# Performance work log

Hardware: AMD Instinct MI355X
Metric: run time of the kernel (lower is better)

The kernel has to match this reference:

```python
import jax, jax.numpy as jnp
import numpy as np

DIM = 1024
HEADS = 16
DIM_HEAD = 64
INNER = HEADS * DIM_HEAD  # 1024
SCALE = DIM_HEAD ** -0.5


def setup_inputs() -> dict:
    key = jax.random.key(0)
    k1, k2, k3, k4 = jax.random.split(key, 4)
    x = jax.random.normal(k1, (2, 2048, DIM), dtype=jnp.float32)
    # nn.Linear(dim, inner*3, bias=False): weight [3*inner, dim]; store transposed [dim, 3*inner]
    w_qkv = jax.random.normal(k2, (DIM, 3 * INNER), dtype=jnp.float32) * (DIM ** -0.5)
    w_out = jax.random.normal(k3, (INNER, DIM), dtype=jnp.float32) * (INNER ** -0.5)
    b_out = jax.random.normal(k4, (DIM,), dtype=jnp.float32) * 0.02
    return {"x": x, "w_qkv": w_qkv, "w_out": w_out, "b_out": b_out}


def _attention(x, w_qkv, w_out, b_out):
    b, n, _ = x.shape
    qkv = x @ w_qkv  # [b, n, 3*inner]
    q_chunk = qkv[..., :INNER]  # NOTE: source bug — q, k, v all come from chunk 0
    def split_heads(t):
        return t.reshape(b, n, HEADS, DIM_HEAD).transpose(0, 2, 1, 3)  # b h n d
    q = split_heads(q_chunk) * SCALE
    k = split_heads(q_chunk)
    v = split_heads(q_chunk)
    dots = jnp.einsum('bhid,bhjd->bhij', q, k)
    mask_value = -jnp.finfo(dots.dtype).max
    causal_mask = jnp.triu(jnp.ones((n, n), dtype=bool), k=1)
    dots = jnp.where(causal_mask, mask_value, dots)
    attn = jax.nn.softmax(dots, axis=-1)
    out = jnp.einsum('bhij,bhjd->bhid', attn, v)
    out = out.transpose(0, 2, 1, 3).reshape(b, n, INNER)
    return out @ w_out + b_out


def reference(x, w_qkv, w_out, b_out):
    return _attention(x, w_qkv, w_out, b_out)
```

## Files before the change

### kernel.cpp

```cpp
#include <hip/hip_runtime.h>
#include <hip/hip_bf16.h>

typedef __attribute__((ext_vector_type(8))) short short8;
typedef __attribute__((ext_vector_type(4))) short bf16x4;
typedef __attribute__((ext_vector_type(4))) float floatx4;

#define MFMA16(a, b, c) __builtin_amdgcn_mfma_f32_16x16x32_bf16((a), (b), (c), 0, 0, 0)

#if defined(__HIP_DEVICE_COMPILE__)
  #if __has_builtin(__builtin_amdgcn_mfma_f32_16x16x16bf16_1k)
    #define MFMA_PV(a, b, c) __builtin_amdgcn_mfma_f32_16x16x16bf16_1k((a), (b), (c), 0, 0, 0)
  #elif __has_builtin(__builtin_amdgcn_mfma_f32_16x16x16_bf16)
    #define MFMA_PV(a, b, c) __builtin_amdgcn_mfma_f32_16x16x16_bf16((a), (b), (c), 0, 0, 0)
  #else
    #error "no 16x16x16 bf16 MFMA builtin found on device pass"
  #endif
#else
  #define MFMA_PV(a, b, c) (c)
#endif

#define SEQ    2048
#define DIMM   1024
#define HEADS  16
#define DHEAD  64
#define ROWS   4096
#define K1 0.18033688011112043f
#define K2 (-34.62468098133512f)


__global__ void cvt_bf16_kernel(const float* __restrict__ src,
                                __hip_bfloat16* __restrict__ dst) {
    const size_t i = (size_t)(blockIdx.x * 256 + threadIdx.x) * 4;
    floatx4 v = *(const floatx4*)(src + i);
    union { bf16x4 s; __hip_bfloat16 h[4]; } u;
#pragma unroll
    for (int j = 0; j < 4; j++) u.h[j] = __float2bfloat16(v[j]);
    *(bf16x4*)(dst + i) = u.s;
}

__global__ __launch_bounds__(256) void transpose_cvt2_kernel(
    const float* __restrict__ W1, __hip_bfloat16* __restrict__ WT1,
    const float* __restrict__ W2, __hip_bfloat16* __restrict__ WT2) {
    __shared__ __hip_bfloat16 tile[64][72];
    const float* W        = blockIdx.z ? W2 : W1;
    __hip_bfloat16* WT    = blockIdx.z ? WT2 : WT1;
    const int ld          = blockIdx.z ? DIMM : 3 * DIMM;
    const int tid = threadIdx.x;
    const int r = tid >> 2, c0 = (tid & 3) * 16;
    const int k0 = blockIdx.x * 64;
    const int n0 = blockIdx.y * 64;
    const float* src = W + (size_t)(k0 + r) * ld + n0 + c0;
    union { short8 v; __hip_bfloat16 h[8]; } a0, a1;
#pragma unroll
    for (int j = 0; j < 8; j++) {
        a0.h[j] = __float2bfloat16(src[j]);
        a1.h[j] = __float2bfloat16(src[8 + j]);
    }
    *(short8*)&tile[r][c0]     = a0.v;
    *(short8*)&tile[r][c0 + 8] = a1.v;
    __syncthreads();
    union { short8 v; __hip_bfloat16 h[8]; } u0, u1;
#pragma unroll
    for (int j = 0; j < 8; j++) {
        u0.h[j] = tile[c0 + j][r];
        u1.h[j] = tile[c0 + 8 + j][r];
    }
    __hip_bfloat16* dst = WT + (size_t)(n0 + r) * 1024 + k0 + c0;
    *(short8*)dst       = u0.v;
    *(short8*)(dst + 8) = u1.v;
}

__global__ __launch_bounds__(256) void transpose_t_kernel(
    const __hip_bfloat16* __restrict__ t,
    __hip_bfloat16* __restrict__ Tt) {
    __shared__ __hip_bfloat16 tile[64][72];
    const int tid = threadIdx.x;
    const int r = tid >> 2, c0 = (tid & 3) * 16;
    const int row0 = blockIdx.x * 64;
    const int col0 = blockIdx.y * 64;
    const __hip_bfloat16* src = t + (size_t)(row0 + r) * DIMM + col0 + c0;
    *(short8*)&tile[r][c0]     = *(const short8*)src;
    *(short8*)&tile[r][c0 + 8] = *(const short8*)(src + 8);
    __syncthreads();
    const int cb = (c0 >> 4) * 4;
    union { short8 v; __hip_bfloat16 h[8]; } u0, u1;
#pragma unroll
    for (int j = 0; j < 8; j++) {
        u0.h[j] = tile[(j >> 2) * 16 + cb + (j & 3)][r];
        u1.h[j] = tile[((j >> 2) + 2) * 16 + cb + (j & 3)][r];
    }
    __hip_bfloat16* dst = Tt + (size_t)(col0 + r) * ROWS + row0 + c0;
    *(short8*)dst       = u0.v;
    *(short8*)(dst + 8) = u1.v;
}

template <typename CT>
__global__ __launch_bounds__(256) void gemm_bf_kernel(
    const __hip_bfloat16* __restrict__ A,
    const __hip_bfloat16* __restrict__ BT,
    const float* __restrict__ bias,
    CT* __restrict__ C, int M, int N, int K) {
    __shared__ __align__(16) __hip_bfloat16 As[2][64][68];
    __shared__ __align__(16) __hip_bfloat16 Bs[2][64][68];

    const int tid  = threadIdx.x;
    const int lane = tid & 63, wid = tid >> 6;
    const int wm   = wid >> 1, wn = wid & 1;
    const int quad = lane >> 4, l15 = lane & 15;
    const int bm = blockIdx.y * 64, bn = blockIdx.x * 64;

    floatx4 acc[2][2];
#pragma unroll
    for (int r = 0; r < 2; r++)
#pragma unroll
        for (int c = 0; c < 2; c++) acc[r][c] = (floatx4){0.f, 0.f, 0.f, 0.f};

    const int sr = tid >> 2, sc = (tid & 3) * 16;
    short8 ra[2], rb[2];
    auto load_tile = [&](int k0) {
        const __hip_bfloat16* pa = A + (size_t)(bm + sr) * K + k0 + sc;
        ra[0] = *(const short8*)pa; ra[1] = *(const short8*)(pa + 8);
        const __hip_bfloat16* pb = BT + (size_t)(bn + sr) * K + k0 + sc;
        rb[0] = *(const short8*)pb; rb[1] = *(const short8*)(pb + 8);
    };
    auto store_tile = [&](int buf) {
        *(short8*)&As[buf][sr][sc]     = ra[0];
        *(short8*)&As[buf][sr][sc + 8] = ra[1];
        *(short8*)&Bs[buf][sr][sc]     = rb[0];
        *(short8*)&Bs[buf][sr][sc + 8] = rb[1];
    };

    load_tile(0);
    store_tile(0);
    if (K > 64) load_tile(64);
    __syncthreads();

    const int nk = K >> 6;
    for (int kb = 0; kb < nk; ++kb) {
        const int buf = kb & 1;
#pragma unroll
        for (int ks = 0; ks < 2; ks++) {
            short8 af[2], bf[2];
#pragma unroll
            for (int r = 0; r < 2; r++)
                af[r] = *(const short8*)&As[buf][wm * 32 + r * 16 + l15][ks * 32 + quad * 8];
#pragma unroll
            for (int c = 0; c < 2; c++)
                bf[c] = *(const short8*)&Bs[buf][wn * 32 + c * 16 + l15][ks * 32 + quad * 8];
#pragma unroll
            for (int r = 0; r < 2; r++)
#pragma unroll
                for (int c = 0; c < 2; c++)
                    acc[r][c] = MFMA16(af[r], bf[c], acc[r][c]);
        }
        if (kb + 1 < nk) store_tile(buf ^ 1);
        if (kb + 2 < nk) load_tile((kb + 2) << 6);
        __syncthreads();
    }

#pragma unroll
    for (int c = 0; c < 2; c++) {
        const int col = bn + wn * 32 + c * 16 + l15;
        const float bv = bias ? bias[col] : 0.f;
#pragma unroll
        for (int r = 0; r < 2; r++) {
            const int row0 = bm + wm * 32 + r * 16 + quad * 4;
#pragma unroll
            for (int i = 0; i < 4; i++) {
                const float v = acc[r][c][i] + bv;
                if constexpr (__is_same(CT, float))
                    C[(size_t)(row0 + i) * N + col] = v;
                else
                    C[(size_t)(row0 + i) * N + col] = __float2bfloat16(v);
            }
        }
    }
}

template <typename AT, typename CT>
__global__ __launch_bounds__(256) void gemm_fp_kernel(
    const AT* __restrict__ A, const float* __restrict__ B,
    const float* __restrict__ bias, CT* __restrict__ C,
    int M, int N, int K, int ldb) {
    __shared__ __align__(16) __hip_bfloat16 As[2][64][40];
    __shared__ __align__(16) __hip_bfloat16 Bs[2][128][40];
    const int tid = threadIdx.x;
    const int lane = tid & 63, wid = tid >> 6;
    const int wm = wid >> 1, wn = wid & 1;
    const int quad = lane >> 4, l15 = lane & 15;
    const int bm = blockIdx.y * 64, bn = blockIdx.x * 128;
    floatx4 acc[2][4];
#pragma unroll
    for (int r = 0; r < 2; r++)
#pragma unroll
        for (int c = 0; c < 4; c++) acc[r][c] = (floatx4){0.f, 0.f, 0.f, 0.f};
    const int a_lr = tid >> 2, a_lc = (tid & 3) * 8;
    const int b_kr = tid & 31, b_nc = (tid >> 5) * 16;
    floatx4 raf0, raf1; short8 rab; floatx4 rb[4];
    auto load_tile = [&](int k0) {
        const AT* pa = A + (size_t)(bm + a_lr) * K + k0 + a_lc;
        if constexpr (__is_same(AT, float)) {
            raf0 = *(const floatx4*)pa; raf1 = *(const floatx4*)(pa + 4);
        } else { rab = *(const short8*)pa; }
        const float* pb = B + (size_t)(k0 + b_kr) * ldb + bn + b_nc;
#pragma unroll
        for (int q = 0; q < 4; q++) rb[q] = *(const floatx4*)(pb + 4 * q);
    };
    auto store_tile = [&](int buf) {
        if constexpr (__is_same(AT, float)) {
            __align__(16) __hip_bfloat16 hh[8];
#pragma unroll
            for (int j = 0; j < 4; j++) {
                hh[j] = __float2bfloat16(raf0[j]); hh[4 + j] = __float2bfloat16(raf1[j]);
            }
            *(short8*)&As[buf][a_lr][a_lc] = *(short8*)&hh[0];
        } else { *(short8*)&As[buf][a_lr][a_lc] = rab; }
#pragma unroll
        for (int q = 0; q < 4; q++)
#pragma unroll
            for (int j = 0; j < 4; j++)
                Bs[buf][b_nc + 4 * q + j][b_kr] = __float2bfloat16(rb[q][j]);
    };
    load_tile(0); store_tile(0);
    if (K > 32) load_tile(32);
    __syncthreads();
    const int nk = K >> 5;
    for (int kb = 0; kb < nk; ++kb) {
        const int buf = kb & 1;
        short8 af[2], bf[4];
#pragma unroll
        for (int r = 0; r < 2; r++)
            af[r] = *(const short8*)&As[buf][wm * 32 + r * 16 + l15][quad * 8];
#pragma unroll
        for (int c = 0; c < 4; c++)
            bf[c] = *(const short8*)&Bs[buf][wn * 64 + c * 16 + l15][quad * 8];
#pragma unroll
        for (int r = 0; r < 2; r++)
#pragma unroll
            for (int c = 0; c < 4; c++)
                acc[r][c] = MFMA16(af[r], bf[c], acc[r][c]);
        if (kb + 1 < nk) store_tile(buf ^ 1);
        if (kb + 2 < nk) load_tile((kb + 2) << 5);
        __syncthreads();
    }
#pragma unroll
    for (int c = 0; c < 4; c++) {
        const int col = bn + wn * 64 + c * 16 + l15;
        const float bv = bias ? bias[col] : 0.f;
#pragma unroll
        for (int r = 0; r < 2; r++) {
            const int row0 = bm + wm * 32 + r * 16 + quad * 4;
#pragma unroll
            for (int i = 0; i < 4; i++) {
                const float v = acc[r][c][i] + bv;
                if constexpr (__is_same(CT, float)) C[(size_t)(row0 + i) * N + col] = v;
                else C[(size_t)(row0 + i) * N + col] = __float2bfloat16(v);
            }
        }
    }
}

__global__ __launch_bounds__(256) void attn_kernel(
    const __hip_bfloat16* __restrict__ T,
    const __hip_bfloat16* __restrict__ Tt,
    __hip_bfloat16* __restrict__ O) {
    __shared__ __align__(16) __hip_bfloat16 Ks[2][64][72];
    __shared__ __align__(16) __hip_bfloat16 Vt[2][64][72];

    const int tid  = threadIdx.x;
    const int lane = tid & 63, wid = tid >> 6;
    const int quad = lane >> 4, l15 = lane & 15;

    const int bx = blockIdx.x;
    const int half = bx >> 9, idx = bx & 511;
    const int g = idx & 15, h = (idx >> 4) & 15, b = idx >> 8;
    const int qt = half ? g : 31 - g;

    const size_t rowbase = (size_t)b * SEQ;
    const int hoff  = h * DHEAD;
    const int qrow0 = qt * 64;

    short8 qf[2];
    {
        const __hip_bfloat16* qp =
            T + (rowbase + qrow0 + wid * 16 + l15) * DIMM + hoff + quad * 8;
        qf[0] = *(const short8*)qp;
        qf[1] = *(const short8*)(qp + 32);
    }

    float l_lane = 0.f;
    floatx4 accO[4];
#pragma unroll
    for (int dt = 0; dt < 4; dt++) accO[dt] = (floatx4){0.f,0.f,0.f,0.f};

    const int sr = tid >> 2;
    const int sc = (tid & 3) * 16;

    short8 rK0, rK1, rV0, rV1;
    auto load_tile = [&](int kt) {
        const __hip_bfloat16* pK = T + (rowbase + kt * 64 + sr) * DIMM + hoff + sc;
        rK0 = *(const short8*)pK; rK1 = *(const short8*)(pK + 8);
        const __hip_bfloat16* pV =
            Tt + (size_t)(hoff + sr) * ROWS + rowbase + kt * 64 + sc;
        rV0 = *(const short8*)pV; rV1 = *(const short8*)(pV + 8);
    };
    auto store_tile = [&](int buf) {
        *(short8*)&Ks[buf][sr][sc]     = rK0;
        *(short8*)&Ks[buf][sr][sc + 8] = rK1;
        *(short8*)&Vt[buf][sr][sc]     = rV0;
        *(short8*)&Vt[buf][sr][sc + 8] = rV1;
    };

    const int last = qt;
    load_tile(0);
    store_tile(0);
    if (last >= 1) load_tile(1);
    __syncthreads();

    for (int kt = 0; kt <= last; ++kt) {
        const int buf = kt & 1;

        floatx4 s[4];
#pragma unroll
        for (int c = 0; c < 4; c++) {
            s[c] = (floatx4){0.f,0.f,0.f,0.f};
#pragma unroll
            for (int ks = 0; ks < 2; ks++) {
                short8 kfr = *(const short8*)&Ks[buf][c * 16 + l15][ks * 32 + quad * 8];
                s[c] = MFMA16(kfr, qf[ks], s[c]);
            }
        }

        bf16x4 pk[4];
        const bool need_mask = (kt == last);
#pragma unroll
        for (int c = 0; c < 4; c++) {
            union { bf16x4 v; __hip_bfloat16 hh[4]; } u;
            float sum = 0.f;
#pragma unroll
            for (int i = 0; i < 4; i++) {
                float v = exp2f(fmaf(s[c][i], K1, K2));
                if (need_mask) {
                    const int key  = kt * 64 + c * 16 + quad * 4 + i;
                    const int qrow = qrow0 + wid * 16 + l15;
                    if (key > qrow) v = 0.f;
                }
                sum += v;
                u.hh[i] = __float2bfloat16(v);
            }
            l_lane += sum;
            pk[c] = u.v;
        }

#pragma unroll
        for (int dt = 0; dt < 4; dt++) {
            union { short8 v; bf16x4 b[2]; } uv, uw;
            uv.v = *(const short8*)&Vt[buf][dt * 16 + l15][quad * 16];
            uw.v = *(const short8*)&Vt[buf][dt * 16 + l15][quad * 16 + 8];
            accO[dt] = MFMA_PV(pk[0], uv.b[0], accO[dt]);
            accO[dt] = MFMA_PV(pk[1], uv.b[1], accO[dt]);
            accO[dt] = MFMA_PV(pk[2], uw.b[0], accO[dt]);
            accO[dt] = MFMA_PV(pk[3], uw.b[1], accO[dt]);
        }

        if (kt < last)      store_tile(buf ^ 1);
        if (kt + 2 <= last) load_tile(kt + 2);
        __syncthreads();
    }

    l_lane += __shfl_xor(l_lane, 16);
    l_lane += __shfl_xor(l_lane, 32);
    float inv[4];
#pragma unroll
    for (int i = 0; i < 4; i++)
        inv[i] = 1.f / __shfl(l_lane, quad * 4 + i, 64);
#pragma unroll
    for (int dt = 0; dt < 4; dt++)
#pragma unroll
        for (int i = 0; i < 4; i++) {
            const size_t row = rowbase + qrow0 + wid * 16 + quad * 4 + i;
            O[row * DIMM + hoff + dt * 16 + l15] =
                __float2bfloat16(accO[dt][i] * inv[i]);
        }
}

extern "C" void kernel_launch(void* const* d_in, const int* in_sizes, int n_in,
                              void* d_out, int out_size, void* d_ws, size_t ws_size,
                              hipStream_t stream) {
    const float* x     = (const float*)d_in[0];
    const float* w_qkv = (const float*)d_in[1];
    const float* w_out = (const float*)d_in[2];
    const float* b_out = (const float*)d_in[3];
    float* out = (float*)d_out;

    __hip_bfloat16* t  = (__hip_bfloat16*)d_out;
    __hip_bfloat16* Tt = (__hip_bfloat16*)((char*)d_out + (8u << 20));
    char* ws = (char*)d_ws;
    __hip_bfloat16* ob = (__hip_bfloat16*)ws;

    if (ws_size >= (size_t)(20u << 20)) {
        __hip_bfloat16* xb  = (__hip_bfloat16*)(ws + (8u  << 20));
        __hip_bfloat16* w1t = (__hip_bfloat16*)(ws + (16u << 20));
        __hip_bfloat16* w2t = (__hip_bfloat16*)(ws + (18u << 20));

        cvt_bf16_kernel<<<4096, 256, 0, stream>>>(x, xb);
        transpose_cvt2_kernel<<<dim3(16, 16, 2), 256, 0, stream>>>(
            w_qkv, w1t, w_out, w2t);

        gemm_bf_kernel<__hip_bfloat16><<<dim3(16, 64), 256, 0, stream>>>(
            xb, w1t, nullptr, t, ROWS, DIMM, DIMM);
        transpose_t_kernel<<<dim3(64, 16), 256, 0, stream>>>(t, Tt);
        attn_kernel<<<dim3(1024), 256, 0, stream>>>(t, Tt, ob);
        gemm_bf_kernel<float><<<dim3(16, 64), 256, 0, stream>>>(
            ob, w2t, b_out, out, ROWS, DIMM, DIMM);
    } else {
        gemm_fp_kernel<float, __hip_bfloat16><<<dim3(8, 64), 256, 0, stream>>>(
            x, w_qkv, nullptr, t, ROWS, DIMM, DIMM, 3 * DIMM);
        transpose_t_kernel<<<dim3(64, 16), 256, 0, stream>>>(t, Tt);
        attn_kernel<<<dim3(1024), 256, 0, stream>>>(t, Tt, ob);
        gemm_fp_kernel<__hip_bfloat16, float><<<dim3(8, 64), 256, 0, stream>>>(
            ob, w_out, b_out, out, ROWS, DIMM, DIMM, DIMM);
    }
}
```

Measured before the change: 164.3 us.

## Stage GEMM tiles via direct global-to-LDS loads with XOR-swizzled layout

Replaces the register-staged double buffer in the bf16 GEMM with global_load_lds direct copies into LDS, issued one tile ahead. The unpadded shared arrays use an XOR swizzle on the 16-byte column chunks to avoid bank conflicts on the MFMA fragment reads. This removes the VGPR round trip and the LDS store instructions, and shrinks shared memory. In exchange there is only one tile of prefetch distance, and correctness depends on the swizzle and the per-wave LDS base offsets matching the builtin's lane-contiguous write pattern.

```diff
diff --git a/kernel.cpp b/kernel.cpp
--- a/kernel.cpp
+++ b/kernel.cpp
@@ -19,6 +19,22 @@
   #define MFMA_PV(a, b, c) (c)
 #endif
 
+#if defined(__HIP_DEVICE_COMPILE__) && __has_builtin(__builtin_amdgcn_global_load_lds)
+  #define HAVE_GLOAD 1
+#else
+  #define HAVE_GLOAD 0
+#endif
+
+__device__ __forceinline__ void gload16(const void* g, void* l) {
+#if HAVE_GLOAD
+    __builtin_amdgcn_global_load_lds(
+        (const __attribute__((address_space(1))) void*)g,
+        (__attribute__((address_space(3))) void*)l, 16, 0, 0);
+#else
+    (void)g; (void)l;
+#endif
+}
+
 #define SEQ    2048
 #define DIMM   1024
 #define HEADS  16
@@ -26,7 +42,6 @@
 #define ROWS   4096
 #define K1 0.18033688011112043f
 #define K2 (-34.62468098133512f)
-
 
 __global__ void cvt_bf16_kernel(const float* __restrict__ src,
                                 __hip_bfloat16* __restrict__ dst) {
@@ -100,8 +115,8 @@
     const __hip_bfloat16* __restrict__ BT,
     const float* __restrict__ bias,
     CT* __restrict__ C, int M, int N, int K) {
-    __shared__ __align__(16) __hip_bfloat16 As[2][64][68];
-    __shared__ __align__(16) __hip_bfloat16 Bs[2][64][68];
+    __shared__ __align__(16) __hip_bfloat16 As[2][64][64];
+    __shared__ __align__(16) __hip_bfloat16 Bs[2][64][64];
 
     const int tid  = threadIdx.x;
     const int lane = tid & 63, wid = tid >> 6;
@@ -115,46 +130,54 @@
 #pragma unroll
         for (int c = 0; c < 2; c++) acc[r][c] = (floatx4){0.f, 0.f, 0.f, 0.f};
 
-    const int sr = tid >> 2, sc = (tid & 3) * 16;
-    short8 ra[2], rb[2];
-    auto load_tile = [&](int k0) {
-        const __hip_bfloat16* pa = A + (size_t)(bm + sr) * K + k0 + sc;
-        ra[0] = *(const short8*)pa; ra[1] = *(const short8*)(pa + 8);
-        const __hip_bfloat16* pb = BT + (size_t)(bn + sr) * K + k0 + sc;
-        rb[0] = *(const short8*)pb; rb[1] = *(const short8*)(pb + 8);
+    const int g_row = wid * 8 + (lane >> 3);
+    const int g_col = (((lane & 7) ^ (lane >> 3)) << 3);
+    const int ldst  = (wid << 10);
+
+    auto stage = [&](int k0, int buf) {
+#if HAVE_GLOAD
+#pragma unroll
+        for (int j = 0; j < 2; j++) {
+            gload16(A + (size_t)(bm + j * 32 + g_row) * K + k0 + g_col,
+                    (char*)&As[buf][0][0] + j * 4096 + ldst);
+            gload16(BT + (size_t)(bn + j * 32 + g_row) * K + k0 + g_col,
+                    (char*)&Bs[buf][0][0] + j * 4096 + ldst);
+        }
+#else
+#pragma unroll
+        for (int j = 0; j < 2; j++) {
+            short8 va = *(const short8*)(A + (size_t)(bm + j * 32 + g_row) * K + k0 + g_col);
+            *(short8*)((char*)&As[buf][0][0] + j * 4096 + ldst + ((lane & 63) << 4)) = va;
+            short8 vb = *(const short8*)(BT + (size_t)(bn + j * 32 + g_row) * K + k0 + g_col);
+            *(short8*)((char*)&Bs[buf][0][0] + j * 4096 + ldst + ((lane & 63) << 4)) = vb;
+        }
+#endif
     };
-    auto store_tile = [&](int buf) {
-        *(short8*)&As[buf][sr][sc]     = ra[0];
-        *(short8*)&As[buf][sr][sc + 8] = ra[1];
-        *(short8*)&Bs[buf][sr][sc]     = rb[0];
-        *(short8*)&Bs[buf][sr][sc + 8] = rb[1];
-    };
-
-    load_tile(0);
-    store_tile(0);
-    if (K > 64) load_tile(64);
+
+    stage(0, 0);
     __syncthreads();
 
+    const int hq = l15 & 7;
     const int nk = K >> 6;
     for (int kb = 0; kb < nk; ++kb) {
         const int buf = kb & 1;
+        if (kb + 1 < nk) stage((kb + 1) << 6, buf ^ 1);
 #pragma unroll
         for (int ks = 0; ks < 2; ks++) {
-            short8 af[2], bf[2];
+            const int col = (((ks << 2) + quad) ^ hq) << 3;
+            short8 af[2], bfr[2];
 #pragma unroll
             for (int r = 0; r < 2; r++)
-                af[r] = *(const short8*)&As[buf][wm * 32 + r * 16 + l15][ks * 32 + quad * 8];
+                af[r] = *(const short8*)&As[buf][wm * 32 + r * 16 + l15][col];
 #pragma unroll
             for (int c = 0; c < 2; c++)
-                bf[c] = *(const short8*)&Bs[buf][wn * 32 + c * 16 + l15][ks * 32 + quad * 8];
+                bfr[c] = *(const short8*)&Bs[buf][wn * 32 + c * 16 + l15][col];
 #pragma unroll
             for (int r = 0; r < 2; r++)
 #pragma unroll
                 for (int c = 0; c < 2; c++)
-                    acc[r][c] = MFMA16(af[r], bf[c], acc[r][c]);
-        }
-        if (kb + 1 < nk) store_tile(buf ^ 1);
-        if (kb + 2 < nk) load_tile((kb + 2) << 6);
+                    acc[r][c] = MFMA16(af[r], bfr[c], acc[r][c]);
+        }
         __syncthreads();
     }
 
```

Measured after the change: 161.7 us. Within noise of the previous version (-1.6%).
